# Optimization experiments

Hardware: AMD Instinct MI355X
Metric: run time of the kernel (lower is better)

The kernel has to match this reference:

```python
import jax, jax.numpy as jnp
import numpy as np

DIM = 256
HEADS = 8
PS = 8  # patch/window size
EPS = 1e-5


def _ln(x, g, b):
    m = x.mean(-1, keepdims=True)
    v = x.var(-1, keepdims=True)
    return (x - m) / jnp.sqrt(v + EPS) * g + b


def setup_inputs() -> dict:
    key = jax.random.key(0)
    ks = jax.random.split(key, 10)
    B, C, H, W = 4, DIM, 256, 256
    s = 0.02
    return {
        "y_lf": jax.random.normal(ks[0], (B, C, H, W), jnp.float32),
        "y_hf": jax.random.normal(ks[1], (B, C, H, W), jnp.float32),
        "g_lf": jnp.ones((C,), jnp.float32),
        "b_lf": jnp.zeros((C,), jnp.float32),
        "g_hf": jnp.ones((C,), jnp.float32),
        "b_hf": jnp.zeros((C,), jnp.float32),
        "Wq": jax.random.normal(ks[2], (C, C), jnp.float32) * s,
        "bq": jnp.zeros((C,), jnp.float32),
        "Wk": jax.random.normal(ks[3], (C, C), jnp.float32) * s,
        "bk": jnp.zeros((C,), jnp.float32),
        "Wv": jax.random.normal(ks[4], (C, C), jnp.float32) * s,
        "bv": jnp.zeros((C,), jnp.float32),
        "Wo": jax.random.normal(ks[5], (C, C), jnp.float32) * s,
        "bo": jnp.zeros((C,), jnp.float32),
    }


def reference(y_lf, y_hf, g_lf, b_lf, g_hf, b_hf, Wq, bq, Wk, bk, Wv, bv, Wo, bo):
    B, C, H, W = y_lf.shape
    ps = PS
    hd = C // HEADS
    nH, nW = H // ps, W // ps

    def win_tokens(x):
        # (B,C,H,W) -> (B*nH*nW, ps*ps, C)
        x = x.reshape(B, C, nH, ps, nW, ps)
        return x.transpose(0, 2, 4, 3, 5, 1).reshape(-1, ps * ps, C)

    lf = win_tokens(y_lf)
    hf = win_tokens(y_hf)  # residual + V source (un-normalized, as in torch code)

    q = _ln(lf, g_lf, b_lf) @ Wq.T + bq
    k = _ln(hf, g_hf, b_hf) @ Wk.T + bk
    v = hf @ Wv.T + bv

    BW, L, _ = q.shape
    q = q.reshape(BW, L, HEADS, hd)
    k = k.reshape(BW, L, HEADS, hd)
    v = v.reshape(BW, L, HEADS, hd)

    scale = 1.0 / np.sqrt(hd).astype(np.float32)
    scores = jnp.einsum('bqhd,bkhd->bhqk', q, k) * scale
    attn = jax.nn.softmax(scores, axis=-1)
    o = jnp.einsum('bhqk,bkhd->bqhd', attn, v).reshape(BW, L, C)
    o = o @ Wo.T + bo + hf  # out_proj + residual

    # window_reverse: (B*nH*nW, ps*ps, C) -> (B,C,H,W)
    o = o.reshape(B, nH, nW, ps, ps, C)
    o = o.transpose(0, 5, 1, 3, 2, 4).reshape(B, C, H, W)
    return o
```

## Files before the change

### kernel.cpp

```cpp
#include <hip/hip_runtime.h>

typedef float  f4     __attribute__((ext_vector_type(4)));
typedef float  f32x4  __attribute__((ext_vector_type(4)));
typedef short  short8 __attribute__((ext_vector_type(8)));
typedef __bf16 bf16x8 __attribute__((ext_vector_type(8)));
typedef int    int4v  __attribute__((ext_vector_type(4)));
typedef unsigned short us4 __attribute__((ext_vector_type(4)));

__device__ __forceinline__ unsigned short f2bf(float f) {
    unsigned int u = __builtin_bit_cast(unsigned int, f);
    u += 0x7FFFu + ((u >> 16) & 1u);
    return (unsigned short)(u >> 16);
}
__device__ __forceinline__ float bf2f(unsigned short h) {
    unsigned int u = ((unsigned int)h) << 16;
    return __builtin_bit_cast(float, u);
}
__device__ __forceinline__ f32x4 mfma_bf16(short8 a, short8 b, f32x4 c) {
    return __builtin_amdgcn_mfma_f32_16x16x32_bf16(
        __builtin_bit_cast(bf16x8, a), __builtin_bit_cast(bf16x8, b), c, 0, 0, 0);
}
__device__ __forceinline__ int cvt_pk_bf16(float lo, float hi) {
    int d;
    asm("v_cvt_pk_bf16_f32 %0, %1, %2" : "=v"(d) : "v"(lo), "v"(hi));
    return d;
}
__device__ __forceinline__ int bperm(int addr, int src) {
    return __builtin_amdgcn_ds_bpermute(addr, src);
}

__global__ void pcaf_precvt(const float* __restrict__ Wq, const float* __restrict__ bq,
                            const float* __restrict__ Wk, const float* __restrict__ bk,
                            const float* __restrict__ Wv, const float* __restrict__ Wo,
                            const float* __restrict__ g_lf, const float* __restrict__ b_lf,
                            const float* __restrict__ g_hf, const float* __restrict__ b_hf,
                            void* __restrict__ ws) {
    const int mat  = blockIdx.x >> 8;
    const int row  = blockIdx.x & 255;
    const int lane = threadIdx.x;
    const float* W = (mat == 0) ? Wq : (mat == 1) ? Wk : (mat == 2) ? Wv : Wo;
    f4 w = *(const f4*)(W + row * 256 + lane * 4);
    f4 wp = w;
    if (mat < 2) {
        const float* g = mat ? g_hf : g_lf;
        f4 gg = *(const f4*)(g + lane * 4);
        wp = w * gg;
    }
    us4 u;
    u[0] = f2bf(wp[0]); u[1] = f2bf(wp[1]); u[2] = f2bf(wp[2]); u[3] = f2bf(wp[3]);
    {
        const int ct   = row >> 4;
        const int l15r = row & 15;
        const int k_   = lane >> 3;
        const int g_   = (lane >> 1) & 3;
        const int e4   = (lane & 1) * 4;
        unsigned short* dst = (unsigned short*)ws + mat * 65536 +
                              (((ct * 8 + k_) * 64) + g_ * 16 + l15r) * 8 + e4;
        *(us4*)dst = u;
    }
    if (mat < 2) {
        const float* b = mat ? b_hf : b_lf;
        f4 bb = *(const f4*)(b + lane * 4);
        float rsum = wp[0] + wp[1] + wp[2] + wp[3];
        float cb   = bb[0] * w[0] + bb[1] * w[1] + bb[2] * w[2] + bb[3] * w[3];
        #pragma unroll
        for (int d = 1; d < 64; d <<= 1) {
            rsum += __shfl_xor(rsum, d);
            cb   += __shfl_xor(cb, d);
        }
        if (lane == 0) {
            float* cons = (float*)((char*)ws + 524288);
            cons[mat * 512 + 2 * row]     = rsum;
            cons[mat * 512 + 2 * row + 1] = cb + (mat ? bk[row] : bq[row]);
        }
    }
}

constexpr int RS  = 528;
constexpr int HWC = 65536;
constexpr int Wd  = 256;
constexpr int OA  = 0;
constexpr int OB  = 33792;
constexpr int OS  = 67584;

struct AccW { f32x4 a[4][2]; };
struct AccT { f32x4 a[2][4]; };

__device__ __forceinline__ AccW gemmW(const char* base,
                                      const unsigned short* __restrict__ Wbw,
                                      int lane, int g, int l15) {
    AccW r;
    f32x4 z = {0.f, 0.f, 0.f, 0.f};
    #pragma unroll
    for (int m = 0; m < 4; ++m) { r.a[m][0] = z; r.a[m][1] = z; }
    #pragma unroll
    for (int half = 0; half < 2; ++half) {
        short8 w0[4], w1[4];
        #pragma unroll
        for (int k = 0; k < 4; ++k) {
            w0[k] = *(const short8*)(Wbw + (half * 4 + k) * 512 + lane * 8);
            w1[k] = *(const short8*)(Wbw + 4096 + (half * 4 + k) * 512 + lane * 8);
        }
        #pragma unroll
        for (int k = 0; k < 4; ++k) {
            #pragma unroll
            for (int m = 0; m < 4; ++m) {
                short8 am = *(const short8*)(base + (16 * m + l15) * RS +
                                             ((half * 4 + k) * 32 + g * 8) * 2);
                r.a[m][0] = mfma_bf16(am, w0[k], r.a[m][0]);
                r.a[m][1] = mfma_bf16(am, w1[k], r.a[m][1]);
            }
        }
    }
    return r;
}

__device__ __forceinline__ AccT gemmWT(const char* base,
                                       const unsigned short* __restrict__ Wbw,
                                       int lane, int g, int l15) {
    AccT r;
    f32x4 z = {0.f, 0.f, 0.f, 0.f};
    #pragma unroll
    for (int n = 0; n < 4; ++n) { r.a[0][n] = z; r.a[1][n] = z; }
    #pragma unroll
    for (int half = 0; half < 2; ++half) {
        short8 w0[4], w1[4];
        #pragma unroll
        for (int k = 0; k < 4; ++k) {
            w0[k] = *(const short8*)(Wbw + (half * 4 + k) * 512 + lane * 8);
            w1[k] = *(const short8*)(Wbw + 4096 + (half * 4 + k) * 512 + lane * 8);
        }
        #pragma unroll
        for (int k = 0; k < 4; ++k) {
            #pragma unroll
            for (int n = 0; n < 4; ++n) {
                short8 tk = *(const short8*)(base + (16 * n + l15) * RS +
                                             ((half * 4 + k) * 32 + g * 8) * 2);
                r.a[0][n] = mfma_bf16(w0[k], tk, r.a[0][n]);
                r.a[1][n] = mfma_bf16(w1[k], tk, r.a[1][n]);
            }
        }
    }
    return r;
}

__device__ __forceinline__ short8 repack4(const int* p0, const int* p1,
                                          int a0, int a1, bool ghi) {
    int4v t;
    #pragma unroll
    for (int j = 0; j < 4; ++j) {
        int ad = (j >> 1) ? a1 : a0;
        int v0 = bperm(ad, p0[j & 1]);
        int v1 = bperm(ad, p1[j & 1]);
        t[j] = ghi ? v1 : v0;
    }
    return __builtin_bit_cast(short8, t);
}

__global__ __attribute__((amdgpu_flat_work_group_size(512, 512), amdgpu_waves_per_eu(3, 4)))
void pcaf17_kernel(
    const float* __restrict__ y_lf, const float* __restrict__ y_hf,
    const float* __restrict__ bv, const float* __restrict__ bo,
    const void* __restrict__ ws, float* __restrict__ out)
{
    __shared__ __align__(16) char sm[68608];

    const unsigned short* wsq = (const unsigned short*)ws;
    const unsigned short* wsk = wsq + 65536;
    const unsigned short* wsv = wsq + 131072;
    const unsigned short* wso = wsq + 196608;
    const float* qc = (const float*)((const char*)ws + 524288);
    const float* kc = qc + 512;

    const int tid = threadIdx.x;
    const int bid = blockIdx.x;
    const int wi  = ((bid & 7) << 9) | (bid >> 3);
    const int bb  = wi >> 10;
    const int nh  = (wi >> 5) & 31;
    const int nw  = wi & 31;
    const long win_base = (long)bb * 256 * HWC + (long)(nh * 8) * Wd + nw * 8;

    const int wave = tid >> 6;
    const int lane = tid & 63;
    const int g    = lane >> 4;
    const int l15  = lane & 15;
    const int c0   = 32 * wave + l15;

    {
        const int half = tid >> 8;
        const int t8   = tid & 255;
        const int pw4  = (t8 & 1) * 4;
        const int c2   = t8 >> 1;
        const float* src = half ? y_hf : y_lf;
        const int dst  = half ? OB : OA;
        const float* gp = src + win_base + (long)(2 * c2) * HWC + pw4;
        #pragma unroll
        for (int hh = 0; hh < 2; ++hh) {
            f4 v0[4], v1[4];
            #pragma unroll
            for (int p = 0; p < 4; ++p) {
                int ph = hh * 4 + p;
                v0[p] = *(const f4*)(gp + ph * Wd);
                v1[p] = *(const f4*)(gp + ph * Wd + HWC);
            }
            #pragma unroll
            for (int p = 0; p < 4; ++p) {
                int ph = hh * 4 + p;
                int tok0 = ph * 8 + pw4;
                #pragma unroll
                for (int j = 0; j < 4; ++j) {
                    unsigned int pk = (unsigned int)f2bf(v0[p][j]) |
                                      ((unsigned int)f2bf(v1[p][j]) << 16);
                    *(unsigned int*)(sm + dst + (tok0 + j) * RS + c2 * 4) = pk;
                }
            }
        }
    }
    __syncthreads();

    {
        const int t = tid >> 3, j = tid & 7;
        #pragma unroll
        for (int pass = 0; pass < 2; ++pass) {
            const int base = pass ? OB : OA;
            float sum = 0.f, ss = 0.f;
            #pragma unroll
            for (int r = 0; r < 4; ++r) {
                short8 raw = *(const short8*)(sm + base + t * RS + (j * 32 + r * 8) * 2);
                #pragma unroll
                for (int e = 0; e < 8; ++e) { float f = bf2f((unsigned short)raw[e]); sum += f; ss += f * f; }
            }
            sum += __shfl_xor(sum, 1); ss += __shfl_xor(ss, 1);
            sum += __shfl_xor(sum, 2); ss += __shfl_xor(ss, 2);
            sum += __shfl_xor(sum, 4); ss += __shfl_xor(ss, 4);
            float mean = sum * (1.f / 256.f);
            float rstd = rsqrtf(ss * (1.f / 256.f) - mean * mean + 1e-5f);
            if (j == 0) {
                float* S = (float*)(sm + OS);
                S[pass * 128 + t]      = mean;
                S[pass * 128 + 64 + t] = rstd;
            }
        }
    }
    __syncthreads();

    const float* S = (const float*)(sm + OS);
    const int  a0  = ((2 * (g & 1)) * 16 + l15) * 4;
    const int  a1  = a0 + 64;
    const bool ghi = (g >> 1) & 1;
    f32x4 z = {0.f, 0.f, 0.f, 0.f};

    short8 vf[2][2];
    {
        AccW vacc = gemmW(sm + OB, wsv + wave * 8192, lane, g, l15);
        float bv0 = bv[c0], bv1 = bv[c0 + 16];
        int vp[4][2][2];
        #pragma unroll
        for (int m = 0; m < 4; ++m) {
            vp[m][0][0] = cvt_pk_bf16(vacc.a[m][0][0] + bv0, vacc.a[m][0][1] + bv0);
            vp[m][0][1] = cvt_pk_bf16(vacc.a[m][0][2] + bv0, vacc.a[m][0][3] + bv0);
            vp[m][1][0] = cvt_pk_bf16(vacc.a[m][1][0] + bv1, vacc.a[m][1][1] + bv1);
            vp[m][1][1] = cvt_pk_bf16(vacc.a[m][1][2] + bv1, vacc.a[m][1][3] + bv1);
        }
        #pragma unroll
        for (int kk = 0; kk < 2; ++kk)
            #pragma unroll
            for (int n2 = 0; n2 < 2; ++n2)
                vf[kk][n2] = repack4(vp[2 * kk][n2], vp[2 * kk + 1][n2], a0, a1, ghi);
    }

    short8 kf[4];
    {
        AccT kacc = gemmWT(sm + OB, wsk + wave * 8192, lane, g, l15);
        float mh[4], rh[4];
        #pragma unroll
        for (int n = 0; n < 4; ++n) {
            mh[n] = S[128 + 16 * n + l15];
            rh[n] = S[192 + 16 * n + l15];
        }
        int kp[2][4][2];
        #pragma unroll
        for (int m = 0; m < 2; ++m) {
            int cb = 32 * wave + 16 * m + 4 * g;
            f4 c0v = *(const f4*)(kc + cb * 2);
            f4 c1v = *(const f4*)(kc + cb * 2 + 4);
            #pragma unroll
            for (int n = 0; n < 4; ++n) {
                float v0 = rh[n] * (kacc.a[m][n][0] - mh[n] * c0v[0]) + c0v[1];
                float v1 = rh[n] * (kacc.a[m][n][1] - mh[n] * c0v[2]) + c0v[3];
                float v2 = rh[n] * (kacc.a[m][n][2] - mh[n] * c1v[0]) + c1v[1];
                float v3 = rh[n] * (kacc.a[m][n][3] - mh[n] * c1v[2]) + c1v[3];
                kp[m][n][0] = cvt_pk_bf16(v0, v1);
                kp[m][n][1] = cvt_pk_bf16(v2, v3);
            }
        }
        #pragma unroll
        for (int x = 0; x < 4; ++x)
            kf[x] = repack4(kp[0][x], kp[1][x], a0, a1, ghi);
    }

    short8 qf[4];
    {
        AccT qacc = gemmWT(sm + OA, wsq + wave * 8192, lane, g, l15);
        const float SCALE = 0.17677669529663687f;
        float ml[4], rl[4];
        #pragma unroll
        for (int n = 0; n < 4; ++n) {
            ml[n] = S[16 * n + l15];
            rl[n] = S[64 + 16 * n + l15];
        }
        int qp[2][4][2];
        #pragma unroll
        for (int m = 0; m < 2; ++m) {
            int cb = 32 * wave + 16 * m + 4 * g;
            f4 c0v = *(const f4*)(qc + cb * 2);
            f4 c1v = *(const f4*)(qc + cb * 2 + 4);
            #pragma unroll
            for (int n = 0; n < 4; ++n) {
                float v0 = (rl[n] * (qacc.a[m][n][0] - ml[n] * c0v[0]) + c0v[1]) * SCALE;
                float v1 = (rl[n] * (qacc.a[m][n][1] - ml[n] * c0v[2]) + c0v[3]) * SCALE;
                float v2 = (rl[n] * (qacc.a[m][n][2] - ml[n] * c1v[0]) + c1v[1]) * SCALE;
                float v3 = (rl[n] * (qacc.a[m][n][3] - ml[n] * c1v[2]) + c1v[3]) * SCALE;
                qp[m][n][0] = cvt_pk_bf16(v0, v1);
                qp[m][n][1] = cvt_pk_bf16(v2, v3);
            }
        }
        #pragma unroll
        for (int x = 0; x < 4; ++x)
            qf[x] = repack4(qp[0][x], qp[1][x], a0, a1, ghi);
    }

    f32x4 o[4][2];
    {
        #pragma unroll
        for (int c = 0; c < 4; ++c) { o[c][0] = z; o[c][1] = z; }

        #pragma unroll
        for (int c = 0; c < 4; ++c) {
            f32x4 stc[4];
            #pragma unroll
            for (int nk = 0; nk < 4; ++nk)
                stc[nk] = mfma_bf16(kf[nk], qf[c], z);

            float mx = stc[0][0];
            #pragma unroll
            for (int nk = 0; nk < 4; ++nk)
                #pragma unroll
                for (int i = 0; i < 4; ++i) mx = fmaxf(mx, stc[nk][i]);
            mx = fmaxf(mx, __shfl_xor(mx, 16));
            mx = fmaxf(mx, __shfl_xor(mx, 32));
            float sum = 0.f;
            #pragma unroll
            for (int nk = 0; nk < 4; ++nk)
                #pragma unroll
                for (int i = 0; i < 4; ++i) {
                    float e = __expf(stc[nk][i] - mx);
                    stc[nk][i] = e;
                    sum += e;
                }
            sum += __shfl_xor(sum, 16);
            sum += __shfl_xor(sum, 32);
            float is = 1.f / sum;

            int pq[4][2];
            #pragma unroll
            for (int nk = 0; nk < 4; ++nk) {
                pq[nk][0] = cvt_pk_bf16(stc[nk][0] * is, stc[nk][1] * is);
                pq[nk][1] = cvt_pk_bf16(stc[nk][2] * is, stc[nk][3] * is);
            }

            #pragma unroll
            for (int kk = 0; kk < 2; ++kk) {
                short8 pf = repack4(pq[2 * kk], pq[2 * kk + 1], a0, a1, ghi);
                o[c][0] = mfma_bf16(pf, vf[kk][0], o[c][0]);
                o[c][1] = mfma_bf16(pf, vf[kk][1], o[c][1]);
            }
        }
    }
    __syncthreads();

    #pragma unroll
    for (int c = 0; c < 4; ++c)
        #pragma unroll
        for (int i = 0; i < 4; ++i) {
            int t = 16 * c + 4 * g + i;
            *(unsigned short*)(sm + OA + t * RS + c0 * 2)        = f2bf(o[c][0][i]);
            *(unsigned short*)(sm + OA + t * RS + (c0 + 16) * 2) = f2bf(o[c][1][i]);
        }
    __syncthreads();

    {
        AccW oacc = gemmW(sm + OA, wso + wave * 8192, lane, g, l15);
        float bo0 = bo[c0], bo1 = bo[c0 + 16];
        #pragma unroll
        for (int n = 0; n < 2; ++n) {
            float bon = n ? bo1 : bo0;
            int cout = c0 + 16 * n;
            #pragma unroll
            for (int m = 0; m < 4; ++m) {
                int tok0 = 16 * m + 4 * g;
                int ph = tok0 >> 3, pw = tok0 & 7;
                f4 ov;
                #pragma unroll
                for (int i = 0; i < 4; ++i) {
                    float rv = bf2f(*(const unsigned short*)(
                        sm + OB + (tok0 + i) * RS + cout * 2));
                    ov[i] = oacc.a[m][n][i] + bon + rv;
                }
                *(f4*)(out + win_base + (long)cout * HWC + ph * Wd + pw) = ov;
            }
        }
    }
}

extern "C" void kernel_launch(void* const* d_in, const int* in_sizes, int n_in,
                              void* d_out, int out_size, void* d_ws, size_t ws_size,
                              hipStream_t stream) {
    (void)in_sizes; (void)n_in; (void)out_size; (void)ws_size;
    const float* y_lf = (const float*)d_in[0];
    const float* y_hf = (const float*)d_in[1];
    const float* g_lf = (const float*)d_in[2];
    const float* b_lf = (const float*)d_in[3];
    const float* g_hf = (const float*)d_in[4];
    const float* b_hf = (const float*)d_in[5];
    const float* Wq   = (const float*)d_in[6];
    const float* bq   = (const float*)d_in[7];
    const float* Wk   = (const float*)d_in[8];
    const float* bk   = (const float*)d_in[9];
    const float* Wv   = (const float*)d_in[10];
    const float* bv   = (const float*)d_in[11];
    const float* Wo   = (const float*)d_in[12];
    const float* bo   = (const float*)d_in[13];
    float* out = (float*)d_out;

    pcaf_precvt<<<dim3(1024), dim3(64), 0, stream>>>(
        Wq, bq, Wk, bk, Wv, Wo, g_lf, b_lf, g_hf, b_hf, d_ws);
    pcaf17_kernel<<<dim3(4096), dim3(512), 0, stream>>>(
        y_lf, y_hf, bv, bo, d_ws, out);
}
```

Baseline: 506.8 us.

## Halve block size so each wave processes two attention heads

Block size drops from 512 to 256 threads, and each of the 4 waves now loops over two heads, covering the QKV projections, attention and output projection. The staging load and LayerNorm statistics loops are re-indexed so fewer threads still cover all channels and tokens. The aim is to cut per-block overhead and barrier cost and to allow more blocks per CU. In exchange, each wave does serial work and holds more registers (two sets of output accumulators), under a waves_per_eu(2,2) hint.

```diff
diff --git a/kernel.cpp b/kernel.cpp
--- a/kernel.cpp
+++ b/kernel.cpp
@@ -157,8 +157,8 @@
     return __builtin_bit_cast(short8, t);
 }
 
-__global__ __attribute__((amdgpu_flat_work_group_size(512, 512), amdgpu_waves_per_eu(3, 4)))
-void pcaf17_kernel(
+__global__ __attribute__((amdgpu_flat_work_group_size(256, 256), amdgpu_waves_per_eu(2, 2)))
+void pcaf18_kernel(
     const float* __restrict__ y_lf, const float* __restrict__ y_hf,
     const float* __restrict__ bv, const float* __restrict__ bo,
     const void* __restrict__ ws, float* __restrict__ out)
@@ -184,34 +184,37 @@
     const int lane = tid & 63;
     const int g    = lane >> 4;
     const int l15  = lane & 15;
-    const int c0   = 32 * wave + l15;
 
     {
-        const int half = tid >> 8;
-        const int t8   = tid & 255;
-        const int pw4  = (t8 & 1) * 4;
-        const int c2   = t8 >> 1;
+        const int half = tid >> 7;
+        const int t7   = tid & 127;
+        const int pw4  = (t7 & 1) * 4;
+        const int c2b  = t7 >> 1;
         const float* src = half ? y_hf : y_lf;
         const int dst  = half ? OB : OA;
-        const float* gp = src + win_base + (long)(2 * c2) * HWC + pw4;
-        #pragma unroll
-        for (int hh = 0; hh < 2; ++hh) {
-            f4 v0[4], v1[4];
-            #pragma unroll
-            for (int p = 0; p < 4; ++p) {
-                int ph = hh * 4 + p;
-                v0[p] = *(const f4*)(gp + ph * Wd);
-                v1[p] = *(const f4*)(gp + ph * Wd + HWC);
-            }
-            #pragma unroll
-            for (int p = 0; p < 4; ++p) {
-                int ph = hh * 4 + p;
-                int tok0 = ph * 8 + pw4;
-                #pragma unroll
-                for (int j = 0; j < 4; ++j) {
-                    unsigned int pk = (unsigned int)f2bf(v0[p][j]) |
-                                      ((unsigned int)f2bf(v1[p][j]) << 16);
-                    *(unsigned int*)(sm + dst + (tok0 + j) * RS + c2 * 4) = pk;
+        #pragma unroll
+        for (int ci = 0; ci < 2; ++ci) {
+            const int c2 = c2b + 64 * ci;
+            const float* gp = src + win_base + (long)(2 * c2) * HWC + pw4;
+            #pragma unroll
+            for (int hb = 0; hb < 2; ++hb) {
+                f4 v0[4], v1[4];
+                #pragma unroll
+                for (int p = 0; p < 4; ++p) {
+                    int ph = hb * 4 + p;
+                    v0[p] = *(const f4*)(gp + ph * Wd);
+                    v1[p] = *(const f4*)(gp + ph * Wd + HWC);
+                }
+                #pragma unroll
+                for (int p = 0; p < 4; ++p) {
+                    int ph = hb * 4 + p;
+                    int tok0 = ph * 8 + pw4;
+                    #pragma unroll
+                    for (int j = 0; j < 4; ++j) {
+                        unsigned int pk = (unsigned int)f2bf(v0[p][j]) |
+                                          ((unsigned int)f2bf(v1[p][j]) << 16);
+                        *(unsigned int*)(sm + dst + (tok0 + j) * RS + c2 * 4) = pk;
+                    }
                 }
             }
         }
@@ -219,10 +222,12 @@
     __syncthreads();
 
     {
-        const int t = tid >> 3, j = tid & 7;
-        #pragma unroll
-        for (int pass = 0; pass < 2; ++pass) {
-            const int base = pass ? OB : OA;
+        const int j = tid & 7;
+        #pragma unroll
+        for (int pass = 0; pass < 4; ++pass) {
+            const int tensor = pass >> 1;
+            const int t = ((pass & 1) << 5) + (tid >> 3);
+            const int base = tensor ? OB : OA;
             float sum = 0.f, ss = 0.f;
             #pragma unroll
             for (int r = 0; r < 4; ++r) {
@@ -237,8 +242,8 @@
             float rstd = rsqrtf(ss * (1.f / 256.f) - mean * mean + 1e-5f);
             if (j == 0) {
                 float* S = (float*)(sm + OS);
-                S[pass * 128 + t]      = mean;
-                S[pass * 128 + 64 + t] = rstd;
+                S[tensor * 128 + t]      = mean;
+                S[tensor * 128 + 64 + t] = rstd;
             }
         }
     }
@@ -250,90 +255,94 @@
     const bool ghi = (g >> 1) & 1;
     f32x4 z = {0.f, 0.f, 0.f, 0.f};
 
-    short8 vf[2][2];
-    {
-        AccW vacc = gemmW(sm + OB, wsv + wave * 8192, lane, g, l15);
-        float bv0 = bv[c0], bv1 = bv[c0 + 16];
-        int vp[4][2][2];
-        #pragma unroll
-        for (int m = 0; m < 4; ++m) {
-            vp[m][0][0] = cvt_pk_bf16(vacc.a[m][0][0] + bv0, vacc.a[m][0][1] + bv0);
-            vp[m][0][1] = cvt_pk_bf16(vacc.a[m][0][2] + bv0, vacc.a[m][0][3] + bv0);
-            vp[m][1][0] = cvt_pk_bf16(vacc.a[m][1][0] + bv1, vacc.a[m][1][1] + bv1);
-            vp[m][1][1] = cvt_pk_bf16(vacc.a[m][1][2] + bv1, vacc.a[m][1][3] + bv1);
-        }
-        #pragma unroll
-        for (int kk = 0; kk < 2; ++kk)
-            #pragma unroll
-            for (int n2 = 0; n2 < 2; ++n2)
-                vf[kk][n2] = repack4(vp[2 * kk][n2], vp[2 * kk + 1][n2], a0, a1, ghi);
-    }
-
-    short8 kf[4];
-    {
-        AccT kacc = gemmWT(sm + OB, wsk + wave * 8192, lane, g, l15);
-        float mh[4], rh[4];
-        #pragma unroll
-        for (int n = 0; n < 4; ++n) {
-            mh[n] = S[128 + 16 * n + l15];
-            rh[n] = S[192 + 16 * n + l15];
-        }
-        int kp[2][4][2];
-        #pragma unroll
-        for (int m = 0; m < 2; ++m) {
-            int cb = 32 * wave + 16 * m + 4 * g;
-            f4 c0v = *(const f4*)(kc + cb * 2);
-            f4 c1v = *(const f4*)(kc + cb * 2 + 4);
+    f32x4 o[2][4][2];
+    #pragma unroll
+    for (int hh = 0; hh < 2; ++hh) {
+        const int head = 2 * wave + hh;
+        const int c0   = 32 * head + l15;
+
+        short8 vf[2][2];
+        {
+            AccW vacc = gemmW(sm + OB, wsv + head * 8192, lane, g, l15);
+            float bv0 = bv[c0], bv1 = bv[c0 + 16];
+            int vp[4][2][2];
+            #pragma unroll
+            for (int m = 0; m < 4; ++m) {
+                vp[m][0][0] = cvt_pk_bf16(vacc.a[m][0][0] + bv0, vacc.a[m][0][1] + bv0);
+                vp[m][0][1] = cvt_pk_bf16(vacc.a[m][0][2] + bv0, vacc.a[m][0][3] + bv0);
+                vp[m][1][0] = cvt_pk_bf16(vacc.a[m][1][0] + bv1, vacc.a[m][1][1] + bv1);
+                vp[m][1][1] = cvt_pk_bf16(vacc.a[m][1][2] + bv1, vacc.a[m][1][3] + bv1);
+            }
+            #pragma unroll
+            for (int kk = 0; kk < 2; ++kk)
+                #pragma unroll
+                for (int n2 = 0; n2 < 2; ++n2)
+                    vf[kk][n2] = repack4(vp[2 * kk][n2], vp[2 * kk + 1][n2], a0, a1, ghi);
+        }
+
+        short8 kf[4];
+        {
+            AccT kacc = gemmWT(sm + OB, wsk + head * 8192, lane, g, l15);
+            float mh[4], rh[4];
             #pragma unroll
             for (int n = 0; n < 4; ++n) {
-                float v0 = rh[n] * (kacc.a[m][n][0] - mh[n] * c0v[0]) + c0v[1];
-                float v1 = rh[n] * (kacc.a[m][n][1] - mh[n] * c0v[2]) + c0v[3];
-                float v2 = rh[n] * (kacc.a[m][n][2] - mh[n] * c1v[0]) + c1v[1];
-                float v3 = rh[n] * (kacc.a[m][n][3] - mh[n] * c1v[2]) + c1v[3];
-                kp[m][n][0] = cvt_pk_bf16(v0, v1);
-                kp[m][n][1] = cvt_pk_bf16(v2, v3);
-            }
-        }
-        #pragma unroll
-        for (int x = 0; x < 4; ++x)
-            kf[x] = repack4(kp[0][x], kp[1][x], a0, a1, ghi);
-    }
-
-    short8 qf[4];
-    {
-        AccT qacc = gemmWT(sm + OA, wsq + wave * 8192, lane, g, l15);
-        const float SCALE = 0.17677669529663687f;
-        float ml[4], rl[4];
-        #pragma unroll
-        for (int n = 0; n < 4; ++n) {
-            ml[n] = S[16 * n + l15];
-            rl[n] = S[64 + 16 * n + l15];
-        }
-        int qp[2][4][2];
-        #pragma unroll
-        for (int m = 0; m < 2; ++m) {
-            int cb = 32 * wave + 16 * m + 4 * g;
-            f4 c0v = *(const f4*)(qc + cb * 2);
-            f4 c1v = *(const f4*)(qc + cb * 2 + 4);
+                mh[n] = S[128 + 16 * n + l15];
+                rh[n] = S[192 + 16 * n + l15];
+            }
+            int kp[2][4][2];
+            #pragma unroll
+            for (int m = 0; m < 2; ++m) {
+                int cb = 32 * head + 16 * m + 4 * g;
+                f4 c0v = *(const f4*)(kc + cb * 2);
+                f4 c1v = *(const f4*)(kc + cb * 2 + 4);
+                #pragma unroll
+                for (int n = 0; n < 4; ++n) {
+                    float v0 = rh[n] * (kacc.a[m][n][0] - mh[n] * c0v[0]) + c0v[1];
+                    float v1 = rh[n] * (kacc.a[m][n][1] - mh[n] * c0v[2]) + c0v[3];
+                    float v2 = rh[n] * (kacc.a[m][n][2] - mh[n] * c1v[0]) + c1v[1];
+                    float v3 = rh[n] * (kacc.a[m][n][3] - mh[n] * c1v[2]) + c1v[3];
+                    kp[m][n][0] = cvt_pk_bf16(v0, v1);
+                    kp[m][n][1] = cvt_pk_bf16(v2, v3);
+                }
+            }
+            #pragma unroll
+            for (int x = 0; x < 4; ++x)
+                kf[x] = repack4(kp[0][x], kp[1][x], a0, a1, ghi);
+        }
+
+        short8 qf[4];
+        {
+            AccT qacc = gemmWT(sm + OA, wsq + head * 8192, lane, g, l15);
+            const float SCALE = 0.17677669529663687f;
+            float ml[4], rl[4];
             #pragma unroll
             for (int n = 0; n < 4; ++n) {
-                float v0 = (rl[n] * (qacc.a[m][n][0] - ml[n] * c0v[0]) + c0v[1]) * SCALE;
-                float v1 = (rl[n] * (qacc.a[m][n][1] - ml[n] * c0v[2]) + c0v[3]) * SCALE;
-                float v2 = (rl[n] * (qacc.a[m][n][2] - ml[n] * c1v[0]) + c1v[1]) * SCALE;
-                float v3 = (rl[n] * (qacc.a[m][n][3] - ml[n] * c1v[2]) + c1v[3]) * SCALE;
-                qp[m][n][0] = cvt_pk_bf16(v0, v1);
-                qp[m][n][1] = cvt_pk_bf16(v2, v3);
-            }
-        }
-        #pragma unroll
-        for (int x = 0; x < 4; ++x)
-            qf[x] = repack4(qp[0][x], qp[1][x], a0, a1, ghi);
-    }
-
-    f32x4 o[4][2];
-    {
-        #pragma unroll
-        for (int c = 0; c < 4; ++c) { o[c][0] = z; o[c][1] = z; }
+                ml[n] = S[16 * n + l15];
+                rl[n] = S[64 + 16 * n + l15];
+            }
+            int qp[2][4][2];
+            #pragma unroll
+            for (int m = 0; m < 2; ++m) {
+                int cb = 32 * head + 16 * m + 4 * g;
+                f4 c0v = *(const f4*)(qc + cb * 2);
+                f4 c1v = *(const f4*)(qc + cb * 2 + 4);
+                #pragma unroll
+                for (int n = 0; n < 4; ++n) {
+                    float v0 = (rl[n] * (qacc.a[m][n][0] - ml[n] * c0v[0]) + c0v[1]) * SCALE;
+                    float v1 = (rl[n] * (qacc.a[m][n][1] - ml[n] * c0v[2]) + c0v[3]) * SCALE;
+                    float v2 = (rl[n] * (qacc.a[m][n][2] - ml[n] * c1v[0]) + c1v[1]) * SCALE;
+                    float v3 = (rl[n] * (qacc.a[m][n][3] - ml[n] * c1v[2]) + c1v[3]) * SCALE;
+                    qp[m][n][0] = cvt_pk_bf16(v0, v1);
+                    qp[m][n][1] = cvt_pk_bf16(v2, v3);
+                }
+            }
+            #pragma unroll
+            for (int x = 0; x < 4; ++x)
+                qf[x] = repack4(qp[0][x], qp[1][x], a0, a1, ghi);
+        }
+
+        #pragma unroll
+        for (int c = 0; c < 4; ++c) { o[hh][c][0] = z; o[hh][c][1] = z; }
 
         #pragma unroll
         for (int c = 0; c < 4; ++c) {
@@ -372,25 +381,32 @@
             #pragma unroll
             for (int kk = 0; kk < 2; ++kk) {
                 short8 pf = repack4(pq[2 * kk], pq[2 * kk + 1], a0, a1, ghi);
-                o[c][0] = mfma_bf16(pf, vf[kk][0], o[c][0]);
-                o[c][1] = mfma_bf16(pf, vf[kk][1], o[c][1]);
+                o[hh][c][0] = mfma_bf16(pf, vf[kk][0], o[hh][c][0]);
+                o[hh][c][1] = mfma_bf16(pf, vf[kk][1], o[hh][c][1]);
             }
         }
     }
     __syncthreads();
 
     #pragma unroll
-    for (int c = 0; c < 4; ++c)
-        #pragma unroll
-        for (int i = 0; i < 4; ++i) {
-            int t = 16 * c + 4 * g + i;
-            *(unsigned short*)(sm + OA + t * RS + c0 * 2)        = f2bf(o[c][0][i]);
-            *(unsigned short*)(sm + OA + t * RS + (c0 + 16) * 2) = f2bf(o[c][1][i]);
-        }
+    for (int hh = 0; hh < 2; ++hh) {
+        const int c0 = 32 * (2 * wave + hh) + l15;
+        #pragma unroll
+        for (int c = 0; c < 4; ++c)
+            #pragma unroll
+            for (int i = 0; i < 4; ++i) {
+                int t = 16 * c + 4 * g + i;
+                *(unsigned short*)(sm + OA + t * RS + c0 * 2)        = f2bf(o[hh][c][0][i]);
+                *(unsigned short*)(sm + OA + t * RS + (c0 + 16) * 2) = f2bf(o[hh][c][1][i]);
+            }
+    }
     __syncthreads();
 
-    {
-        AccW oacc = gemmW(sm + OA, wso + wave * 8192, lane, g, l15);
+    #pragma unroll
+    for (int hh = 0; hh < 2; ++hh) {
+        const int head = 2 * wave + hh;
+        const int c0   = 32 * head + l15;
+        AccW oacc = gemmW(sm + OA, wso + head * 8192, lane, g, l15);
         float bo0 = bo[c0], bo1 = bo[c0 + 16];
         #pragma unroll
         for (int n = 0; n < 2; ++n) {
@@ -435,6 +451,6 @@
 
     pcaf_precvt<<<dim3(1024), dim3(64), 0, stream>>>(
         Wq, bq, Wk, bk, Wv, Wo, g_lf, b_lf, g_hf, b_hf, d_ws);
-    pcaf17_kernel<<<dim3(4096), dim3(512), 0, stream>>>(
+    pcaf18_kernel<<<dim3(4096), dim3(256), 0, stream>>>(
         y_lf, y_hf, bv, bo, d_ws, out);
 }
```

Measured after the change: 653.4 us. 1.29x slower.
